# Kernel optimization log

Hardware: AMD Instinct MI355X
Metric: run time of the kernel (lower is better)

## Reference

```python
import jax, jax.numpy as jnp
import numpy as np

N_ROI = 1024
N_CLASS = 21      # num_classes + 1
APP_DIM = 1024
D_F = 128
N_REL = 16
DIM_K = 64
DIM_G = 64


def loc2bbox(src, loc):
    # src, loc: [M,4] with (y0,x0,y1,x1) / (dy,dx,dh,dw)
    h = src[:, 2] - src[:, 0]
    w = src[:, 3] - src[:, 1]
    cy = src[:, 0] + 0.5 * h
    cx = src[:, 1] + 0.5 * w
    ncy = loc[:, 0] * h + cy
    ncx = loc[:, 1] * w + cx
    nh = jnp.exp(loc[:, 2]) * h
    nw = jnp.exp(loc[:, 3]) * w
    return jnp.stack([ncy - 0.5 * nh, ncx - 0.5 * nw,
                      ncy + 0.5 * nh, ncx + 0.5 * nw], axis=1)


def rank_embedding(n, feat_dim, wave_len=1000.0):
    rank = jnp.arange(n, dtype=jnp.float32)[:, None]
    fr = jnp.arange(feat_dim // 2, dtype=jnp.float32)
    dim_mat = 1.0 / (wave_len ** (fr / (feat_dim / 2.0)))
    mul = rank * dim_mat[None, :]
    return jnp.concatenate([jnp.sin(mul), jnp.cos(mul)], axis=-1)  # [n, feat_dim]


def positional_embedding(f_g, dim_g, wave_len=1000.0):
    # f_g: [N,4]; replicates the repo's PositionalEmbedding exactly
    x_min, y_min, x_max, y_max = jnp.split(f_g, 4, axis=1)  # [N,1] each
    cx = (x_min + x_max) * 0.5
    cy = (y_min + y_max) * 0.5
    w = (x_max - x_min) + 1.0
    h = (y_max - y_min) + 1.0
    dx = jnp.log(jnp.maximum(jnp.abs((cx - cx.T) / w), 1e-3))
    dy = jnp.log(jnp.maximum(jnp.abs((cy - cy.T) / h), 1e-3))
    dw = jnp.log(w / w.T)
    dh = jnp.log(h / h.T)
    pos = jnp.stack([dx, dy, dw, dh], axis=-1)               # [N,N,4]
    fr = jnp.arange(dim_g // 8, dtype=jnp.float32)
    dim_mat = 1.0 / (wave_len ** (fr / (dim_g / 8.0)))       # [dim_g/8]
    mul = (100.0 * pos)[..., None] * dim_mat                 # [N,N,4,dim_g/8]
    mul = mul.reshape(pos.shape[0], pos.shape[1], -1)
    return jnp.concatenate([jnp.sin(mul), jnp.cos(mul)], axis=-1)  # [N,N,dim_g]


def setup_inputs():
    key = jax.random.key(0)
    ks = jax.random.split(key, 16)
    yx = jax.random.uniform(ks[0], (N_ROI, 2), minval=0.0, maxval=500.0)
    hw = jax.random.uniform(ks[1], (N_ROI, 2), minval=16.0, maxval=128.0)
    sample_roi = jnp.concatenate([yx, yx + hw], axis=1)      # valid (y0,x0,y1,x1)
    roi_cls_loc = jax.random.normal(ks[2], (N_ROI, N_CLASS * 4)) * 0.5
    roi_score = jax.random.normal(ks[3], (N_ROI, N_CLASS))
    # force no background argmax -> nonzero() filter keeps all N (static shapes)
    roi_score = roi_score.at[:, 0].add(-10.0)
    appearance_features = jax.random.normal(ks[4], (N_ROI, APP_DIM))
    size = jnp.array([600, 800], dtype=jnp.int32)
    s = 0.02
    rank_w = jax.random.normal(ks[5], (APP_DIM, D_F)) * s
    rank_b = jnp.zeros((D_F,), jnp.float32)
    feat_w = jax.random.normal(ks[6], (APP_DIM, D_F)) * s
    feat_b = jnp.zeros((D_F,), jnp.float32)
    logit_w = jax.random.normal(ks[7], (APP_DIM, 1)) * s
    logit_b = jnp.zeros((1,), jnp.float32)
    wg_w = jax.random.normal(ks[8], (N_REL, DIM_G)) * s
    wg_b = jnp.full((N_REL,), 0.1, jnp.float32)  # keep some geo weights > 0
    wk_w = jax.random.normal(ks[9], (N_REL, D_F, DIM_K)) * s
    wk_b = jnp.zeros((N_REL, DIM_K), jnp.float32)
    wq_w = jax.random.normal(ks[10], (N_REL, D_F, DIM_K)) * s
    wq_b = jnp.zeros((N_REL, DIM_K), jnp.float32)
    wv_w = jax.random.normal(ks[11], (N_REL, D_F, DIM_K)) * s
    wv_b = jnp.zeros((N_REL, DIM_K), jnp.float32)
    return {"sample_roi": sample_roi, "roi_cls_loc": roi_cls_loc,
            "roi_score": roi_score, "appearance_features": appearance_features,
            "size": size,
            "rank_w": rank_w, "rank_b": rank_b, "feat_w": feat_w, "feat_b": feat_b,
            "logit_w": logit_w, "logit_b": logit_b,
            "wg_w": wg_w, "wg_b": wg_b, "wk_w": wk_w, "wk_b": wk_b,
            "wq_w": wq_w, "wq_b": wq_b, "wv_w": wv_w, "wv_b": wv_b}


def reference(sample_roi, roi_cls_loc, roi_score, appearance_features, size,
              rank_w, rank_b, feat_w, feat_b, logit_w, logit_b,
              wg_w, wg_b, wk_w, wk_b, wq_w, wq_b, wv_w, wv_b):
    n = sample_roi.shape[0]
    size_f = size.astype(jnp.float32)
    # loc denormalization (mean = 0)
    std = jnp.tile(jnp.array([0.1, 0.1, 0.2, 0.2], jnp.float32), N_CLASS)
    loc = (roi_cls_loc * std).reshape(-1, 4)                  # [N*21,4]
    roi_rep = jnp.broadcast_to(sample_roi[:, None, :], (n, N_CLASS, 4)).reshape(-1, 4)
    cls_bbox = loc2bbox(roi_rep, loc).reshape(n, N_CLASS, 4)
    # replicates original's clamp on class-strided slices of the [N,21,4] view
    cls_bbox = cls_bbox.at[:, 0::2].set(jnp.clip(cls_bbox[:, 0::2], 0.0, size_f[0]))
    cls_bbox = cls_bbox.at[:, 1::2].set(jnp.clip(cls_bbox[:, 1::2], 0.0, size_f[1]))
    prob_all = jax.nn.softmax(roi_score, axis=1)
    prob = jnp.max(prob_all, axis=-1)
    prob_argmax = jnp.argmax(prob_all, axis=-1)
    cls_bbox = cls_bbox[jnp.arange(n), prob_argmax]           # [N,4]
    # background filter; inputs guarantee all foreground -> static size n
    nz = jnp.nonzero(prob_argmax, size=n, fill_value=0)[0]
    prob_argmax = prob_argmax[nz]
    prob = prob[nz]
    cls_bbox = cls_bbox[nz]
    feats = appearance_features[nz]
    order = jnp.argsort(-prob)                                # descending
    sorted_prob = prob[order]
    sorted_cls_bboxes = cls_bbox[order]
    sorted_labels = prob_argmax[order]
    sorted_features = feats[order]
    nms_rank = rank_embedding(n, APP_DIM) @ rank_w + rank_b   # [N,D_F]
    emb_feat = sorted_features @ feat_w + feat_b + nms_rank   # [N,D_F]
    pos_emb = positional_embedding(sorted_cls_bboxes, DIM_G)  # [N,N,DIM_G]
    # 16 independent RelationUnits, batched as heads h
    w_g = jax.nn.relu(jnp.einsum('mng,hg->hmn', pos_emb, wg_w) + wg_b[:, None, None])
    k = jnp.einsum('nd,hdk->hnk', emb_feat, wk_w) + wk_b[:, None, :]
    q = jnp.einsum('nd,hdk->hnk', emb_feat, wq_w) + wq_b[:, None, :]
    v = jnp.einsum('nd,hdk->hnk', emb_feat, wv_w) + wv_b[:, None, :]
    # scaled_dot[m,n] = k_m . q_n (row m is 'key', softmax over n) per original
    scores = jnp.einsum('hmk,hnk->hmn', k, q) / np.sqrt(DIM_K).astype(np.float32)
    w_mn = jax.nn.softmax(jnp.log(jnp.maximum(w_g, 1e-6)) + scores, axis=-1)
    rel = jnp.einsum('hmn,hnk->hmk', w_mn, v)                 # [H,N,K]
    rel = rel.transpose(1, 0, 2).reshape(n, N_REL * DIM_K) + sorted_features
    s1 = jax.nn.sigmoid(rel @ logit_w + logit_b).reshape(-1)
    nms_scores = s1 * sorted_prob
    return nms_scores, sorted_labels - 1, sorted_cls_bboxes
```

## Files before the change

kernel.cpp:

```cpp
#include <hip/hip_runtime.h>
#include <hip/hip_bf16.h>
#include <math.h>

typedef unsigned long long u64;
typedef unsigned int u32;
typedef __hip_bfloat16 bf16;

#define N 1024
#define NCLS 21
#define APP 1024
#define DF 128
#define NH 16
#define DK 64
#define NS 2

typedef __attribute__((ext_vector_type(8))) short short8v;
typedef __attribute__((ext_vector_type(4))) float float4v;
union U4S8 { uint4 u; short8v s; };

__device__ __forceinline__ float b2f(bf16 x) { return __bfloat162float(x); }
__device__ __forceinline__ ushort f2bu(float x) { bf16 b = __float2bfloat16(x); return *(ushort*)&b; }
__device__ __forceinline__ float bu2f(ushort u) { return __uint_as_float(((uint)u) << 16); }

__global__ void k_prep(const float* __restrict__ roi, const float* __restrict__ cls_loc,
                       const float* __restrict__ score, const int* __restrict__ size,
                       const float* __restrict__ wgw,
                       float* __restrict__ prob, int* __restrict__ label,
                       float* __restrict__ bbox, u64* __restrict__ keys,
                       ushort* __restrict__ wgwb)
{
    int i = blockIdx.x * 256 + threadIdx.x;
    if (i >= N) return;
    wgwb[i] = f2bu(wgw[i]);

    float s[NCLS];
    float mx = -1e30f; int am = 0;
    for (int c = 0; c < NCLS; c++) {
        s[c] = score[i * NCLS + c];
        if (s[c] > mx) { mx = s[c]; am = c; }
    }
    float sum = 0.f;
    for (int c = 0; c < NCLS; c++) sum += expf(s[c] - mx);
    float p = 1.0f / sum;

    float y0 = roi[i*4+0], x0 = roi[i*4+1];
    float y1 = roi[i*4+2], x1 = roi[i*4+3];
    float hh = y1 - y0, ww = x1 - x0;
    float cy = y0 + 0.5f * hh, cx = x0 + 0.5f * ww;
    float l0 = cls_loc[i*84 + am*4 + 0] * 0.1f;
    float l1 = cls_loc[i*84 + am*4 + 1] * 0.1f;
    float l2 = cls_loc[i*84 + am*4 + 2] * 0.2f;
    float l3 = cls_loc[i*84 + am*4 + 3] * 0.2f;
    float ncy = l0 * hh + cy, ncx = l1 * ww + cx;
    float nh = expf(l2) * hh, nw = expf(l3) * ww;
    float b0 = ncy - 0.5f * nh, b1 = ncx - 0.5f * nw;
    float b2v = ncy + 0.5f * nh, b3 = ncx + 0.5f * nw;
    float lim = ((am & 1) == 0) ? (float)size[0] : (float)size[1];
    b0  = fminf(fmaxf(b0, 0.f), lim);
    b1  = fminf(fmaxf(b1, 0.f), lim);
    b2v = fminf(fmaxf(b2v, 0.f), lim);
    b3  = fminf(fmaxf(b3, 0.f), lim);
    prob[i] = p; label[i] = am;
    bbox[i*4+0] = b0; bbox[i*4+1] = b1; bbox[i*4+2] = b2v; bbox[i*4+3] = b3;
    keys[i] = ((u64)(0xFFFFFFFFu - __float_as_uint(p)) << 32) | (u32)i;
}

__global__ void __launch_bounds__(256) k_rank(
        const u64* __restrict__ keys, const float* __restrict__ prob,
        const int* __restrict__ label, const float* __restrict__ bbox,
        int* __restrict__ order, float* __restrict__ sprob,
        float* __restrict__ sbbox, float* __restrict__ sgeo,
        float* __restrict__ out)
{
    __shared__ u64 sk[N];
    int t = threadIdx.x;
    for (int j = t; j < N; j += 256) sk[j] = keys[j];
    __syncthreads();
    int il = t >> 2, q = t & 3;
    int i = blockIdx.x * 64 + il;
    u64 my = sk[i];
    int r = 0;
    int j0 = q * 256;
    #pragma unroll 8
    for (int j = j0; j < j0 + 256; j++) r += (sk[j] < my) ? 1 : 0;
    r += __shfl_xor(r, 1, 64);
    r += __shfl_xor(r, 2, 64);
    if (q == 0) {
        order[r] = i;
        sprob[r] = prob[i];
        float b0 = bbox[i*4+0], b1 = bbox[i*4+1], b2 = bbox[i*4+2], b3 = bbox[i*4+3];
        sbbox[r*4+0] = b0; sbbox[r*4+1] = b1; sbbox[r*4+2] = b2; sbbox[r*4+3] = b3;
        sgeo[r*4+0] = (b0 + b2) * 0.5f;
        sgeo[r*4+1] = (b1 + b3) * 0.5f;
        sgeo[r*4+2] = __logf(b2 - b0 + 1.0f);
        sgeo[r*4+3] = __logf(b3 - b1 + 1.0f);
        out[N + r] = (float)(label[i] - 1);
        out[2*N + r*4 + 0] = b0;
        out[2*N + r*4 + 1] = b1;
        out[2*N + r*4 + 2] = b2;
        out[2*N + r*4 + 3] = b3;
    }
}

__global__ void __launch_bounds__(256) k_geoemb(
        const int* __restrict__ order, const float* __restrict__ app,
        const float* __restrict__ feat_w, const float* __restrict__ rank_w,
        float* __restrict__ part,
        const float* __restrict__ sbbox, const float* __restrict__ sgeo,
        const ushort* __restrict__ wgwb,
        const float* __restrict__ wgb, bf16* __restrict__ lw)
{
    __shared__ __align__(16) char smem[33024];
    int bx = blockIdx.x, t = threadIdx.x;
    int w = t >> 6, l = t & 63, l15 = l & 15, quad = l >> 4;

    if (bx >= 256) {
        uint (*sOut)[516] = (uint(*)[516])smem;
        int m = bx - 256;

        float4 mg = *(const float4*)&sgeo[m*4];
        float4 mb = *(const float4*)&sbbox[m*4];
        float wm = mb.z - mb.x + 1.0f, hm = mb.w - mb.y + 1.0f;

        float sC  = (quad == 0) ? mg.x : (quad == 1) ? mg.y : 0.0f;
        float sM  = ((quad & 1) == 0) ? 1e-3f * wm : 1e-3f * hm;
        float sL  = ((quad & 1) == 0) ? mg.z : mg.w;
        float sSg = (quad < 2) ? 100.0f : -100.0f;

        U4S8 Bg0, Bg1;
        const uint4* wg4 = (const uint4*)wgwb;
        Bg0.u = wg4[l15*8 + quad];
        Bg1.u = wg4[l15*8 + 4 + quad];
        float bias = wgb[l15];

        const float dmt[8] = { 1.0f, 0.42169650342f, 0.177827941f, 0.0749894209f,
                               0.0316227766f, 0.01333521432f, 0.00562341325f, 0.00237137371f };

        #pragma unroll 4
        for (int mt2 = 0; mt2 < 16; mt2++) {
            int n = mt2*64 + w*16 + l15;
            float valn = sgeo[n*4 + quad];
            float lg = __logf(fmaxf(fabsf(sC - valn), sM));
            float lv = (quad < 2) ? lg : valn;
            float P  = sSg * (lv - sL);

            U4S8 Af0, Af1;
            #pragma unroll
            for (int j = 0; j < 4; j++) {
                float s0, c0, s1, c1;
                __sincosf(P * dmt[2*j],     &s0, &c0);
                __sincosf(P * dmt[2*j + 1], &s1, &c1);
                ((uint*)&Af0)[j] = (uint)f2bu(s0) | ((uint)f2bu(s1) << 16);
                ((uint*)&Af1)[j] = (uint)f2bu(c0) | ((uint)f2bu(c1) << 16);
            }

            float4v c = (float4v){0.f, 0.f, 0.f, 0.f};
            c = __builtin_amdgcn_mfma_f32_16x16x32_bf16(Af0.s, Bg0.s, c, 0, 0, 0);
            c = __builtin_amdgcn_mfma_f32_16x16x32_bf16(Af1.s, Bg1.s, c, 0, 0, 0);
            float v0 = __logf(fmaxf(c[0] + bias, 1e-6f));
            float v1 = __logf(fmaxf(c[1] + bias, 1e-6f));
            float v2 = __logf(fmaxf(c[2] + bias, 1e-6f));
            float v3 = __logf(fmaxf(c[3] + bias, 1e-6f));
            int pb = mt2*32 + w*8 + quad*2;
            sOut[l15][pb]     = (uint)f2bu(v0) | ((uint)f2bu(v1) << 16);
            sOut[l15][pb + 1] = (uint)f2bu(v2) | ((uint)f2bu(v3) << 16);
        }
        __syncthreads();
        uint* lwu = (uint*)lw;
        #pragma unroll
        for (int it = 0; it < 8; it++) {
            int idx = t + it * 256;
            int hh = idx >> 7, col4 = idx & 127;
            uint4 val = *(const uint4*)&sOut[hh][col4*4];
            *(uint4*)&lwu[((size_t)hh << 19) + ((size_t)m << 9) + col4*4] = val;
        }
    } else {
        ushort (*sA)[72] = (ushort(*)[72])smem;
        ushort (*sW)[72] = (ushort(*)[72])(smem + 9216);
        int* sOrd = (int*)(smem + 27648);
        int idx0 = bx;
        int rt = idx0 & 15, dg = (idx0 >> 4) & 7, ph = idx0 >> 7;
        int r0 = rt * 64;
        if (t < 64) sOrd[t] = order[r0 + t];
        __syncthreads();

        const float* Wsrc = ph ? rank_w : feat_w;
        float4v acc[8];
        #pragma unroll
        for (int nb = 0; nb < 8; nb++) acc[nb] = (float4v){0.f, 0.f, 0.f, 0.f};

        for (int dc = dg * 2; dc < dg * 2 + 2; dc++) {
            int d0 = dc * 64;
            #pragma unroll
            for (int it = 0; it < 32; it++) {
                int idx = t + it * 256;
                int d = idx >> 7, c = idx & 127;
                sW[c][d] = f2bu(Wsrc[(size_t)(d0 + d) * 128 + c]);
            }
            if (ph == 0) {
                #pragma unroll
                for (int it = 0; it < 16; it++) {
                    int idx = t + it * 256;
                    int r = idx >> 6, d = idx & 63;
                    sA[r][d] = f2bu(app[(size_t)sOrd[r] * 1024 + d0 + d]);
                }
            } else {
                #pragma unroll
                for (int it = 0; it < 16; it++) {
                    int idx = t + it * 256;
                    int r = idx >> 6, d = idx & 63;
                    int dgl = d0 + d;
                    float irow = (float)(r0 + r);
                    float val;
                    if (dgl < 512) val = __sinf(irow * exp2f(-(float)dgl * 0.019464422f));
                    else           val = __cosf(irow * exp2f(-(float)(dgl - 512) * 0.019464422f));
                    sA[r][d] = f2bu(val);
                }
            }
            __syncthreads();
            U4S8 Af0, Af1;
            Af0.u = *(uint4*)&sA[w*16 + l15][quad*8];
            Af1.u = *(uint4*)&sA[w*16 + l15][32 + quad*8];
            #pragma unroll
            for (int nb = 0; nb < 8; nb++) {
                U4S8 Bf0, Bf1;
                Bf0.u = *(uint4*)&sW[nb*16 + l15][quad*8];
                Bf1.u = *(uint4*)&sW[nb*16 + l15][32 + quad*8];
                acc[nb] = __builtin_amdgcn_mfma_f32_16x16x32_bf16(Af0.s, Bf0.s, acc[nb], 0, 0, 0);
                acc[nb] = __builtin_amdgcn_mfma_f32_16x16x32_bf16(Af1.s, Bf1.s, acc[nb], 0, 0, 0);
            }
            __syncthreads();
        }
        #pragma unroll
        for (int reg = 0; reg < 4; reg++) {
            int row = r0 + w*16 + quad*4 + reg;
            #pragma unroll
            for (int nb = 0; nb < 8; nb++)
                part[(((size_t)ph * 8 + dg) * 1024 + row) * 128 + nb*16 + l15] = acc[nb][reg];
        }
    }
}

__global__ void k_embsum(const float* __restrict__ part,
                         const float* __restrict__ feat_b, const float* __restrict__ rank_b,
                         bf16* __restrict__ embb)
{
    int gid = blockIdx.x * 256 + threadIdx.x;
    int c = gid & 127;
    float acc = feat_b[c] + rank_b[c];
    #pragma unroll
    for (int p8 = 0; p8 < 16; p8++) acc += part[(size_t)p8 * 131072 + gid];
    embb[gid] = __float2bfloat16(acc);
}

__global__ void __launch_bounds__(256) k_qkv2(
        const bf16* __restrict__ embb,
        const float* __restrict__ wq, const float* __restrict__ bq,
        const float* __restrict__ wk, const float* __restrict__ bk,
        const float* __restrict__ wv, const float* __restrict__ bv,
        bf16* __restrict__ q, bf16* __restrict__ k, bf16* __restrict__ v)
{
    __shared__ ushort sWt[64][136];
    int t = threadIdx.x;
    int rt = blockIdx.x, h = blockIdx.y, mat = blockIdx.z;
    const float* W  = (mat == 0) ? wq : (mat == 1) ? wk : wv;
    const float* Bb = (mat == 0) ? bq : (mat == 1) ? bk : bv;
    bf16* Out       = (mat == 0) ? q  : (mat == 1) ? k  : v;

    #pragma unroll
    for (int i = 0; i < 32; i++) {
        int idx = t + i * 256;
        int d = idx >> 6, kk = idx & 63;
        sWt[kk][d] = f2bu(W[((size_t)h * 128 + d) * 64 + kk]);
    }
    int w = t >> 6, l = t & 63, l15 = l & 15, quad = l >> 4;
    float biasv[4];
    #pragma unroll
    for (int nb = 0; nb < 4; nb++) biasv[nb] = Bb[h * 64 + nb*16 + l15];
    __syncthreads();

    U4S8 Bf[4][4];
    #pragma unroll
    for (int nb = 0; nb < 4; nb++)
        #pragma unroll
        for (int kc = 0; kc < 4; kc++)
            Bf[nb][kc].u = *(uint4*)&sWt[nb*16 + l15][kc*32 + quad*8];

    const uint4* A4 = (const uint4*)embb;
    int r0 = rt * 128 + w * 32;
    ushort* outu = (ushort*)Out;
    for (int mb = 0; mb < 2; mb++) {
        int arow = r0 + mb*16 + l15;
        U4S8 Af[4];
        #pragma unroll
        for (int kc = 0; kc < 4; kc++) Af[kc].u = A4[(size_t)arow * 16 + kc*4 + quad];
        float4v acc[4];
        #pragma unroll
        for (int nb = 0; nb < 4; nb++) acc[nb] = (float4v){0.f, 0.f, 0.f, 0.f};
        #pragma unroll
        for (int kc = 0; kc < 4; kc++)
            #pragma unroll
            for (int nb = 0; nb < 4; nb++)
                acc[nb] = __builtin_amdgcn_mfma_f32_16x16x32_bf16(Af[kc].s, Bf[nb][kc].s, acc[nb], 0, 0, 0);
        #pragma unroll
        for (int reg = 0; reg < 4; reg++) {
            int orow = r0 + mb*16 + quad*4 + reg;
            #pragma unroll
            for (int nb = 0; nb < 4; nb++)
                outu[((size_t)h * N + orow) * 64 + nb*16 + l15] = f2bu(acc[nb][reg] + biasv[nb]);
        }
    }
}

__global__ void __launch_bounds__(256) k_attn4(
        const bf16* __restrict__ q, const bf16* __restrict__ kmat,
        const bf16* __restrict__ v, const bf16* __restrict__ lw,
        bf16* __restrict__ opartb, float* __restrict__ mpart, float* __restrict__ zpart)
{
    __shared__ uint sQu[64][36];
    __shared__ uint sVtu[64][36];
    __shared__ uint slwu[64][36];
    __shared__ uint sPu[4][16][36];

    int t = threadIdx.x;
    int mt = blockIdx.x, h = blockIdx.y, ns = blockIdx.z;
    int m0 = mt * 64;
    int w = t >> 6, l = t & 63, l15 = l & 15, quad = l >> 4;

    U4S8 kf0, kf1;
    {
        const uint4* k4 = (const uint4*)kmat;
        size_t krow = ((size_t)h * N + m0 + w*16 + l15) * 8;
        kf0.u = k4[krow + quad];
        kf1.u = k4[krow + 4 + quad];
    }

    float4v O[4];
    float M[4], Z[4];
    #pragma unroll
    for (int i = 0; i < 4; i++) {
        O[i] = (float4v){0.f, 0.f, 0.f, 0.f};
        M[i] = -1e30f; Z[i] = 0.f;
    }

    const uint* qsrc = (const uint*)q;
    const uint* vsrc = (const uint*)v;
    const uint* lwsrc = (const uint*)lw;

    for (int tile = ns * (16/NS); tile < (ns + 1) * (16/NS); tile++) {
        int n0 = tile * 64;
        #pragma unroll
        for (int i = 0; i < 8; i++) {
            int idx = t + i * 256;
            int nj = idx >> 5, kp = idx & 31;
            sQu[nj][kp] = qsrc[((size_t)h * N + n0 + nj) * 32 + kp];
        }
        #pragma unroll
        for (int i = 0; i < 4; i++) {
            int idx = t + i * 256;
            int a = idx & 31, nh2 = idx >> 5;
            uint g0 = vsrc[((size_t)h * N + n0 + 2*nh2) * 32 + a];
            uint g1 = vsrc[((size_t)h * N + n0 + 2*nh2 + 1) * 32 + a];
            sVtu[2*a][nh2]     = (g0 & 0xFFFFu) | (g1 << 16);
            sVtu[2*a + 1][nh2] = (g0 >> 16) | (g1 & 0xFFFF0000u);
        }
        #pragma unroll
        for (int i = 0; i < 8; i++) {
            int idx = t + i * 256;
            int mi = idx >> 5, np = idx & 31;
            slwu[mi][np] = lwsrc[((size_t)h << 19) + ((size_t)(m0 + mi) << 9) + (n0 >> 1) + np];
        }
        __syncthreads();

        float4v S[4];
        #pragma unroll
        for (int nb = 0; nb < 4; nb++) {
            U4S8 bq0, bq1;
            bq0.u = *(uint4*)&sQu[nb*16 + l15][quad*4];
            bq1.u = *(uint4*)&sQu[nb*16 + l15][16 + quad*4];
            float4v zz = (float4v){0.f, 0.f, 0.f, 0.f};
            float4v p0 = __builtin_amdgcn_mfma_f32_16x16x32_bf16(kf0.s, bq0.s, zz, 0, 0, 0);
            S[nb] = __builtin_amdgcn_mfma_f32_16x16x32_bf16(kf1.s, bq1.s, p0, 0, 0, 0);
        }
        ushort* pRow[4];
        #pragma unroll
        for (int r = 0; r < 4; r++) pRow[r] = (ushort*)&sPu[w][quad*4 + r][0];
        #pragma unroll
        for (int r = 0; r < 4; r++) {
            int mi = w*16 + quad*4 + r;
            float sv[4];
            #pragma unroll
            for (int nb = 0; nb < 4; nb++) {
                int col = nb*16 + l15;
                uint lu = slwu[mi][col >> 1];
                float lv = (col & 1) ? __uint_as_float(lu & 0xFFFF0000u)
                                     : __uint_as_float(lu << 16);
                sv[nb] = S[nb][r] * 0.125f + lv;
            }
            float rm = fmaxf(fmaxf(sv[0], sv[1]), fmaxf(sv[2], sv[3]));
            #pragma unroll
            for (int off = 1; off < 16; off <<= 1)
                rm = fmaxf(rm, __shfl_xor(rm, off, 64));
            float newM = fmaxf(M[r], rm);
            float pr[4], rs = 0.f;
            #pragma unroll
            for (int nb = 0; nb < 4; nb++) {
                pr[nb] = __expf(sv[nb] - newM);
                rs += pr[nb];
            }
            #pragma unroll
            for (int off = 1; off < 16; off <<= 1)
                rs += __shfl_xor(rs, off, 64);
            float sc = __expf(M[r] - newM);
            M[r] = newM;
            Z[r] = Z[r] * sc + rs;
            #pragma unroll
            for (int kvb = 0; kvb < 4; kvb++) O[kvb][r] *= sc;
            #pragma unroll
            for (int nb = 0; nb < 4; nb++)
                pRow[r][nb*16 + l15] = f2bu(pr[nb]);
        }
        {
            U4S8 ap0, ap1;
            ap0.u = *(uint4*)&sPu[w][l15][quad*4];
            ap1.u = *(uint4*)&sPu[w][l15][16 + quad*4];
            #pragma unroll
            for (int kvb = 0; kvb < 4; kvb++) {
                U4S8 bv0, bv1;
                bv0.u = *(uint4*)&sVtu[kvb*16 + l15][quad*4];
                bv1.u = *(uint4*)&sVtu[kvb*16 + l15][16 + quad*4];
                O[kvb] = __builtin_amdgcn_mfma_f32_16x16x32_bf16(ap0.s, bv0.s, O[kvb], 0, 0, 0);
                O[kvb] = __builtin_amdgcn_mfma_f32_16x16x32_bf16(ap1.s, bv1.s, O[kvb], 0, 0, 0);
            }
        }
        __syncthreads();
    }

    ushort* ob = (ushort*)opartb;
    #pragma unroll
    for (int r = 0; r < 4; r++) {
        int m = m0 + w*16 + quad*4 + r;
        size_t row = ((size_t)ns * NH + h) * N + m;
        #pragma unroll
        for (int kvb = 0; kvb < 4; kvb++)
            ob[row * 64 + kvb*16 + l15] = f2bu(O[kvb][r]);
        if (l15 == 0) { mpart[row] = M[r]; zpart[row] = Z[r]; }
    }
}

__global__ void __launch_bounds__(128) k_final2(
        const bf16* __restrict__ opartb, const float* __restrict__ mpart,
        const float* __restrict__ zpart, const int* __restrict__ order,
        const float* __restrict__ app, const float* __restrict__ lw,
        const float* __restrict__ lb, const float* __restrict__ sprob,
        float* __restrict__ out)
{
    __shared__ float sWgt[NH][NS];
    __shared__ float sInvZ[NH];
    __shared__ float red[2];
    int m = blockIdx.x, t = threadIdx.x;
    if (t < NH) {
        int h = t;
        float Ms[NS], Mg = -1e30f;
        #pragma unroll
        for (int ns = 0; ns < NS; ns++) {
            Ms[ns] = mpart[(size_t)ns * 16384 + h * 1024 + m];
            Mg = fmaxf(Mg, Ms[ns]);
        }
        float Zt = 0.f;
        #pragma unroll
        for (int ns = 0; ns < NS; ns++) {
            float wgt = __expf(Ms[ns] - Mg);
            sWgt[h][ns] = wgt;
            Zt += zpart[(size_t)ns * 16384 + h * 1024 + m] * wgt;
        }
        sInvZ[h] = 1.0f / Zt;
    }
    __syncthreads();
    int o = order[m];
    const ushort* ob = (const ushort*)opartb;
    float s = 0.f;
    for (int j = t; j < APP; j += 128) {
        int hh = j >> 6, kk = j & 63;
        size_t base = ((size_t)hh * 1024 + m) * 64 + kk;
        float val = 0.f;
        #pragma unroll
        for (int ns = 0; ns < NS; ns++)
            val += bu2f(ob[(size_t)ns * 1048576 + base]) * sWgt[hh][ns];
        float rv = val * sInvZ[hh] + app[o * APP + j];
        s += rv * lw[j];
    }
    #pragma unroll
    for (int off = 32; off > 0; off >>= 1) s += __shfl_down(s, off, 64);
    if ((t & 63) == 0) red[t >> 6] = s;
    __syncthreads();
    if (t == 0) {
        float tot = red[0] + red[1] + lb[0];
        float s1 = 1.0f / (1.0f + expf(-tot));
        out[m] = s1 * sprob[m];
    }
}

extern "C" void kernel_launch(void* const* d_in, const int* in_sizes, int n_in,
                              void* d_out, int out_size, void* d_ws, size_t ws_size,
                              hipStream_t stream)
{
    const float* roi      = (const float*)d_in[0];
    const float* cls_loc  = (const float*)d_in[1];
    const float* score    = (const float*)d_in[2];
    const float* app      = (const float*)d_in[3];
    const int*   size     = (const int*)d_in[4];
    const float* rank_w   = (const float*)d_in[5];
    const float* rank_b   = (const float*)d_in[6];
    const float* feat_w   = (const float*)d_in[7];
    const float* feat_b   = (const float*)d_in[8];
    const float* logit_w  = (const float*)d_in[9];
    const float* logit_b  = (const float*)d_in[10];
    const float* wg_w     = (const float*)d_in[11];
    const float* wg_b     = (const float*)d_in[12];
    const float* wk_w     = (const float*)d_in[13];
    const float* wk_b     = (const float*)d_in[14];
    const float* wq_w     = (const float*)d_in[15];
    const float* wq_b     = (const float*)d_in[16];
    const float* wv_w     = (const float*)d_in[17];
    const float* wv_b     = (const float*)d_in[18];
    float* out = (float*)d_out;

    char* ws = (char*)d_ws;
    float* prob  = (float*)(ws + 0);
    int*   label = (int*)  (ws + 4096);
    float* bbox  = (float*)(ws + 8192);
    u64*   keys  = (u64*)  (ws + 24576);
    int*   order = (int*)  (ws + 32768);
    float* sprob = (float*)(ws + 36864);
    float* sbbox = (float*)(ws + 40960);
    bf16*  embb  = (bf16*) (ws + 57344);
    ushort* wgwb = (ushort*)(ws + 1048576);
    float* sgeo  = (float*)(ws + 1052672);
    bf16*  q     = (bf16*) (ws + 8970240);
    bf16*  k     = (bf16*) (ws + 11067392);
    bf16*  v     = (bf16*) (ws + 13164544);
    bf16*  lwbuf = (bf16*) (ws + 17358848);
    float* part  = (float*)(ws + 50913280);
    bf16*  opartb= (bf16*) (ws + 67690496);
    float* mpart = (float*)(ws + 84467712);
    float* zpart = (float*)(ws + 84729856);

    k_prep<<<4, 256, 0, stream>>>(roi, cls_loc, score, size, wg_w, prob, label, bbox, keys, wgwb);
    k_rank<<<16, 256, 0, stream>>>(keys, prob, label, bbox, order, sprob, sbbox, sgeo, out);
    k_geoemb<<<1280, 256, 0, stream>>>(order, app, feat_w, rank_w, part,
                                       sbbox, sgeo, wgwb, wg_b, lwbuf);
    k_embsum<<<512, 256, 0, stream>>>(part, feat_b, rank_b, embb);
    k_qkv2<<<dim3(8, 16, 3), 256, 0, stream>>>(embb, wq_w, wq_b, wk_w, wk_b, wv_w, wv_b, q, k, v);
    k_attn4<<<dim3(16, 16, NS), 256, 0, stream>>>(q, k, v, lwbuf, opartb, mpart, zpart);
    k_final2<<<1024, 128, 0, stream>>>(opartb, mpart, zpart, order, app, logit_w, logit_b, sprob, out);
}
```

Measured before the change: 168.3 us.

## Prefetch next tile's Q, V and log-weight into registers during compute

```diff
diff --git a/kernel.cpp b/kernel.cpp
--- a/kernel.cpp
+++ b/kernel.cpp
@@ -347,30 +347,61 @@
     const uint* vsrc = (const uint*)v;
     const uint* lwsrc = (const uint*)lw;
 
-    for (int tile = ns * (16/NS); tile < (ns + 1) * (16/NS); tile++) {
-        int n0 = tile * 64;
+    uint rq[8], rv0[4], rv1[4], rlw[8];
+    int tile0 = ns * (16/NS), tileE = tile0 + (16/NS);
+
+    {
+        int n0 = tile0 * 64;
         #pragma unroll
         for (int i = 0; i < 8; i++) {
-            int idx = t + i * 256;
-            int nj = idx >> 5, kp = idx & 31;
-            sQu[nj][kp] = qsrc[((size_t)h * N + n0 + nj) * 32 + kp];
+            int idx = t + i * 256; int nj = idx >> 5, kp = idx & 31;
+            rq[i] = qsrc[((size_t)h * N + n0 + nj) * 32 + kp];
         }
         #pragma unroll
         for (int i = 0; i < 4; i++) {
-            int idx = t + i * 256;
-            int a = idx & 31, nh2 = idx >> 5;
-            uint g0 = vsrc[((size_t)h * N + n0 + 2*nh2) * 32 + a];
-            uint g1 = vsrc[((size_t)h * N + n0 + 2*nh2 + 1) * 32 + a];
-            sVtu[2*a][nh2]     = (g0 & 0xFFFFu) | (g1 << 16);
-            sVtu[2*a + 1][nh2] = (g0 >> 16) | (g1 & 0xFFFF0000u);
+            int idx = t + i * 256; int a = idx & 31, nh2 = idx >> 5;
+            rv0[i] = vsrc[((size_t)h * N + n0 + 2*nh2) * 32 + a];
+            rv1[i] = vsrc[((size_t)h * N + n0 + 2*nh2 + 1) * 32 + a];
         }
         #pragma unroll
         for (int i = 0; i < 8; i++) {
-            int idx = t + i * 256;
-            int mi = idx >> 5, np = idx & 31;
-            slwu[mi][np] = lwsrc[((size_t)h << 19) + ((size_t)(m0 + mi) << 9) + (n0 >> 1) + np];
-        }
-        __syncthreads();
+            int idx = t + i * 256; int mi = idx >> 5, np = idx & 31;
+            rlw[i] = lwsrc[((size_t)h << 19) + ((size_t)(m0 + mi) << 9) + (n0 >> 1) + np];
+        }
+        #pragma unroll
+        for (int i = 0; i < 8; i++) { int idx = t + i * 256; sQu[idx >> 5][idx & 31] = rq[i]; }
+        #pragma unroll
+        for (int i = 0; i < 4; i++) {
+            int idx = t + i * 256; int a = idx & 31, nh2 = idx >> 5;
+            sVtu[2*a][nh2]     = (rv0[i] & 0xFFFFu) | (rv1[i] << 16);
+            sVtu[2*a + 1][nh2] = (rv0[i] >> 16) | (rv1[i] & 0xFFFF0000u);
+        }
+        #pragma unroll
+        for (int i = 0; i < 8; i++) { int idx = t + i * 256; slwu[idx >> 5][idx & 31] = rlw[i]; }
+    }
+    __syncthreads();
+
+    for (int tile = tile0; tile < tileE; tile++) {
+        bool more = (tile + 1 < tileE);
+        if (more) {
+            int n0 = (tile + 1) * 64;
+            #pragma unroll
+            for (int i = 0; i < 8; i++) {
+                int idx = t + i * 256; int nj = idx >> 5, kp = idx & 31;
+                rq[i] = qsrc[((size_t)h * N + n0 + nj) * 32 + kp];
+            }
+            #pragma unroll
+            for (int i = 0; i < 4; i++) {
+                int idx = t + i * 256; int a = idx & 31, nh2 = idx >> 5;
+                rv0[i] = vsrc[((size_t)h * N + n0 + 2*nh2) * 32 + a];
+                rv1[i] = vsrc[((size_t)h * N + n0 + 2*nh2 + 1) * 32 + a];
+            }
+            #pragma unroll
+            for (int i = 0; i < 8; i++) {
+                int idx = t + i * 256; int mi = idx >> 5, np = idx & 31;
+                rlw[i] = lwsrc[((size_t)h << 19) + ((size_t)(m0 + mi) << 9) + (n0 >> 1) + np];
+            }
+        }
 
         float4v S[4];
         #pragma unroll
@@ -434,6 +465,20 @@
             }
         }
         __syncthreads();
+
+        if (more) {
+            #pragma unroll
+            for (int i = 0; i < 8; i++) { int idx = t + i * 256; sQu[idx >> 5][idx & 31] = rq[i]; }
+            #pragma unroll
+            for (int i = 0; i < 4; i++) {
+                int idx = t + i * 256; int a = idx & 31, nh2 = idx >> 5;
+                sVtu[2*a][nh2]     = (rv0[i] & 0xFFFFu) | (rv1[i] << 16);
+                sVtu[2*a + 1][nh2] = (rv0[i] >> 16) | (rv1[i] & 0xFFFF0000u);
+            }
+            #pragma unroll
+            for (int i = 0; i < 8; i++) { int idx = t + i * 256; slwu[idx >> 5][idx & 31] = rlw[i]; }
+            __syncthreads();
+        }
     }
 
     ushort* ob = (ushort*)opartb;
```

New measurement: 167.9 us. About the same (-0.3%).
